# Optimization experiments

Hardware: AMD Instinct MI355X
Metric: run time of the kernel (lower is better)

Reference implementation:

```python
import jax, jax.numpy as jnp
import numpy as np

NUM_LAYERS = 3
INPUT_SIZE = 64
EMB = 128
NUM_CAT = 128          # must equal EMB for the W_e_proj assignment to shape-check
NUM_QUERIES = 1
INIT_SCALE = 0.02
KERNEL_PARAM = 1.0     # referenced-but-undefined in source; standard alpha=1
B = 16
N = 2048
D = INPUT_SIZE + 2 * EMB                 # 320, transformer embedding dim
F_IN = INPUT_SIZE + NUM_CAT + EMB        # 320, raw input feature dim


def setup_inputs() -> dict:
    key = jax.random.key(0)
    k = jax.random.split(key, 6)
    x = jax.random.normal(k[0], (B, F_IN, N), dtype=jnp.float32)
    embedding_matrix = jax.random.normal(k[1], (EMB, NUM_CAT), dtype=jnp.float32)
    W_Q = jax.random.normal(k[2], (NUM_LAYERS, 1, D, D), dtype=jnp.float32) * INIT_SCALE
    W_K = jax.random.normal(k[3], (NUM_LAYERS, 1, D, D), dtype=jnp.float32) * INIT_SCALE
    W_V = jax.random.normal(k[4], (NUM_LAYERS, 1, D, D), dtype=jnp.float32) * INIT_SCALE
    P = jax.random.normal(k[5], (NUM_LAYERS, 1, D, D), dtype=jnp.float32) * INIT_SCALE
    return {"x": x, "embedding_matrix": embedding_matrix,
            "W_Q": W_Q, "W_K": W_K, "W_V": W_V, "P": P}


def _build_We(embedding_matrix):
    W = jnp.zeros((D, F_IN), dtype=embedding_matrix.dtype)
    W = W.at[:INPUT_SIZE, :INPUT_SIZE].set(jnp.eye(INPUT_SIZE, dtype=W.dtype))
    W = W.at[D - EMB:, F_IN - EMB:].set(jnp.eye(EMB, dtype=W.dtype))
    # rows [input_size : D-emb], cols [input_size : F-num_categories]
    W = W.at[INPUT_SIZE:D - EMB, INPUT_SIZE:F_IN - NUM_CAT].set(embedding_matrix)
    return W


def reference(x, embedding_matrix, W_Q, W_K, W_V, P):
    W = _build_We(embedding_matrix)
    h = jnp.einsum('df,bfn->bdn', W, x)                        # [B, D, N]
    for nl in range(NUM_LAYERS):
        key = h[:, :, :-NUM_QUERIES]                           # include_query=False
        value = key
        query = h
        n_context = key.shape[-1]
        Q = jnp.einsum('id,bdm->bim', W_Q[nl, 0], query)       # [B, D, N]
        K = jnp.einsum('id,bdn->bin', W_K[nl, 0], key)         # [B, D, M]
        V = jnp.einsum('id,bdn->bin', W_V[nl, 0], value)       # [B, D, M]
        # linear kernel scores
        scores = KERNEL_PARAM * jnp.einsum('bim,bin->bmn', Q, K)  # [B, N, M]
        attn = jnp.einsum('bin,bmn->bim', V, scores) / n_context  # [B, D, N]
        h = h + jnp.einsum('ji,bim->bjm', P[nl, 0], attn)
    f = h[:, -EMB:, :]                                         # [B, EMB, N] (squeeze no-op for B>1)
    logits = jnp.einsum('bdn,dc->bnc', f, embedding_matrix)    # [B, N, C]
    predictions = jax.nn.softmax(logits, axis=-1)
    return logits, predictions
```

## Files before the change

kernel.cpp:

```cpp
#include <hip/hip_runtime.h>
#include <math.h>

typedef long long ll;
typedef unsigned int uint;
typedef unsigned short ushort;
typedef __attribute__((ext_vector_type(4))) float f32x4;
typedef __attribute__((ext_vector_type(8))) short bf16x8;

#define SZ 102400LL
#define RS 40960LL

__device__ inline void split2(float v, ushort& h, ushort& l)
{
    uint u = __float_as_uint(v);
    uint uh = u + (0x7FFFu + ((u >> 16) & 1u));
    h = (ushort)(uh >> 16);
    float hf = __uint_as_float((uint)h << 16);
    float d = v - hf;
    uint ud = __float_as_uint(d);
    l = (ushort)((ud + (0x7FFFu + ((ud >> 16) & 1u))) >> 16);
}
__device__ inline float us2f(ushort h, ushort l)
{
    return __uint_as_float((uint)h << 16) + __uint_as_float((uint)l << 16);
}

__global__ __launch_bounds__(256) void sp_k(
    const float* __restrict__ Wq, const float* __restrict__ Wk,
    const float* __restrict__ Wv, const float* __restrict__ P,
    const float* __restrict__ emb,
    ushort* __restrict__ WqTs, ushort* __restrict__ WkTs, ushort* __restrict__ WvTs,
    ushort* __restrict__ Ps, ushort* __restrict__ embs, ushort* __restrict__ embTs,
    float* __restrict__ q0)
{
    int bid = blockIdx.x, tid = threadIdx.x;
    if (bid < 225) {
        int m = bid / 25, t = bid % 25;
        const float* mats[3] = {Wq, Wk, Wv};
        ushort* dsts[3] = {WqTs, WkTs, WvTs};
        const float* src = mats[m / 3] + (ll)(m % 3) * SZ;
        ushort* dst = dsts[m / 3] + (ll)(m % 3) * SZ;
        int r0 = (t / 5) * 64, c0 = (t % 5) * 64;
        __shared__ float T[64][65];
        #pragma unroll
        for (int s = 0; s < 4; ++s) {
            int idx = s * 256 + tid;
            int r = idx >> 4, cq = (idx & 15) * 4;
            *(float4*)&T[r][cq] = *(const float4*)(src + (ll)(r0 + r) * 320 + c0 + cq);
        }
        __syncthreads();
        {
            int c = tid >> 2, kq = (tid & 3) * 16;
            bf16x8 h0, h1, l0, l1;
            #pragma unroll
            for (int u = 0; u < 8; ++u) {
                ushort h, l;
                split2(T[kq + u][c], h, l);     h0[u] = (short)h; l0[u] = (short)l;
                split2(T[kq + 8 + u][c], h, l); h1[u] = (short)h; l1[u] = (short)l;
            }
            ushort* dh = dst + (ll)(c0 + c) * 320 + r0 + kq;
            *(bf16x8*)dh = h0; *(bf16x8*)(dh + 8) = h1;
            *(bf16x8*)(dh + 3 * SZ) = l0; *(bf16x8*)(dh + 3 * SZ + 8) = l1;
        }
    } else if (bid < 375) {
        ll off = (ll)(bid - 225) * 2048 + tid * 8;
        float4 v0 = *(const float4*)(P + off);
        float4 v1 = *(const float4*)(P + off + 4);
        float vals[8] = {v0.x,v0.y,v0.z,v0.w,v1.x,v1.y,v1.z,v1.w};
        bf16x8 hv, lv;
        #pragma unroll
        for (int u = 0; u < 8; ++u) { ushort h,l; split2(vals[u],h,l);
                                      hv[u]=(short)h; lv[u]=(short)l; }
        *(bf16x8*)(Ps + off) = hv;
        *(bf16x8*)(Ps + off + 3 * SZ) = lv;
    } else if (bid < 383) {
        ll off = (ll)(bid - 375) * 2048 + tid * 8;
        float4 v0 = *(const float4*)(emb + off);
        float4 v1 = *(const float4*)(emb + off + 4);
        float vals[8] = {v0.x,v0.y,v0.z,v0.w,v1.x,v1.y,v1.z,v1.w};
        bf16x8 hv, lv;
        #pragma unroll
        for (int u = 0; u < 8; ++u) { ushort h,l; split2(vals[u],h,l);
                                      hv[u]=(short)h; lv[u]=(short)l; }
        *(bf16x8*)(embs + off) = hv;
        *(bf16x8*)(embs + off + 16384) = lv;
    } else if (bid < 387) {
        int t = bid - 383;
        int r0 = (t >> 1) * 64, c0 = (t & 1) * 64;
        __shared__ float T[64][65];
        {
            int r = tid >> 2, cq = (tid & 3) * 4;
            *(float4*)&T[r][cq]      = *(const float4*)(emb + (ll)(r0 + r) * 128 + c0 + cq);
            *(float4*)&T[r][cq + 16] = *(const float4*)(emb + (ll)(r0 + r) * 128 + c0 + cq + 16);
            *(float4*)&T[r][cq + 32] = *(const float4*)(emb + (ll)(r0 + r) * 128 + c0 + cq + 32);
            *(float4*)&T[r][cq + 48] = *(const float4*)(emb + (ll)(r0 + r) * 128 + c0 + cq + 48);
        }
        __syncthreads();
        {
            int c = tid >> 2, kq = (tid & 3) * 16;
            bf16x8 h0, h1, l0, l1;
            #pragma unroll
            for (int u = 0; u < 8; ++u) {
                ushort h, l;
                split2(T[kq + u][c], h, l);     h0[u]=(short)h; l0[u]=(short)l;
                split2(T[kq + 8 + u][c], h, l); h1[u]=(short)h; l1[u]=(short)l;
            }
            ushort* dh = embTs + (ll)(c0 + c) * 128 + r0 + kq;
            *(bf16x8*)dh = h0; *(bf16x8*)(dh + 8) = h1;
            *(bf16x8*)(dh + 16384) = l0; *(bf16x8*)(dh + 16384 + 8) = l1;
        }
    } else {
        ll base = (ll)(bid - 387) * 2048;
        #pragma unroll
        for (int s = 0; s < 8; ++s) {
            ll id = base + s * 256 + tid;
            int c = (int)(id / 320), i = (int)(id % 320);
            q0[id] = (i >= 192) ? emb[(ll)(i - 192) * 128 + c] : 0.f;
        }
    }
}

__global__ __launch_bounds__(256) void gram_mfma_k(const float* __restrict__ x,
                                                   float* __restrict__ part)
{
    int flat = blockIdx.x;
    int swz = (flat & 7) * 120 + (flat >> 3);
    int b = swz / 60;
    int rr = swz - b * 60;
    int p = rr / 15, t = rr - p * 15;
    int ti = 0, rem = t;
    while (rem >= 5 - ti) { rem -= 5 - ti; ++ti; }
    int tj = ti + rem;
    int i0 = ti * 64, j0 = tj * 64;
    bool diag = (ti == tj);
    const float* X = x + (ll)b * 320 * 2048;
    __shared__ __align__(16) ushort Ah[64 * 40], Al_[64 * 40], Bh[64 * 40], Bl_[64 * 40];
    int tid = threadIdx.x;
    int wv = tid >> 6, lane = tid & 63;
    int lr = lane & 15, kb = (lane >> 4) * 8;
    int cr = tid >> 2, ck = (tid & 3) * 8;
    f32x4 hh[4], hl[4], lh[4];
    f32x4 zz = {0.f, 0.f, 0.f, 0.f};
    #pragma unroll
    for (int f = 0; f < 4; ++f) { hh[f] = zz; hl[f] = zz; lh[f] = zz; }
    const ushort* BhS = diag ? Ah : Bh;
    const ushort* BlS = diag ? Al_ : Bl_;

    for (int it = 0; it < 16; ++it) {
        int kg0 = p * 512 + it * 32;
        {
            const float* src = X + (ll)(i0 + cr) * 2048 + kg0 + ck;
            float4 v0 = *(const float4*)src;
            float4 v1 = *(const float4*)(src + 4);
            float vals[8] = {v0.x,v0.y,v0.z,v0.w,v1.x,v1.y,v1.z,v1.w};
            if (kg0 + ck + 7 >= 2047) {
                #pragma unroll
                for (int u = 0; u < 8; ++u) if (kg0 + ck + u >= 2047) vals[u] = 0.f;
            }
            bf16x8 hv, lv;
            #pragma unroll
            for (int u = 0; u < 8; ++u) { ushort h, l; split2(vals[u], h, l);
                                          hv[u] = (short)h; lv[u] = (short)l; }
            *(bf16x8*)&Ah[cr * 40 + ck] = hv;
            *(bf16x8*)&Al_[cr * 40 + ck] = lv;
        }
        if (!diag) {
            const float* src = X + (ll)(j0 + cr) * 2048 + kg0 + ck;
            float4 v0 = *(const float4*)src;
            float4 v1 = *(const float4*)(src + 4);
            float vals[8] = {v0.x,v0.y,v0.z,v0.w,v1.x,v1.y,v1.z,v1.w};
            if (kg0 + ck + 7 >= 2047) {
                #pragma unroll
                for (int u = 0; u < 8; ++u) if (kg0 + ck + u >= 2047) vals[u] = 0.f;
            }
            bf16x8 hv, lv;
            #pragma unroll
            for (int u = 0; u < 8; ++u) { ushort h, l; split2(vals[u], h, l);
                                          hv[u] = (short)h; lv[u] = (short)l; }
            *(bf16x8*)&Bh[cr * 40 + ck] = hv;
            *(bf16x8*)&Bl_[cr * 40 + ck] = lv;
        }
        __syncthreads();
        bf16x8 ah = *(const bf16x8*)&Ah[(wv * 16 + lr) * 40 + kb];
        bf16x8 al = *(const bf16x8*)&Al_[(wv * 16 + lr) * 40 + kb];
        #pragma unroll
        for (int f = 0; f < 4; ++f) {
            bf16x8 bh_ = *(const bf16x8*)&BhS[(f * 16 + lr) * 40 + kb];
            bf16x8 bl_ = *(const bf16x8*)&BlS[(f * 16 + lr) * 40 + kb];
            hh[f] = __builtin_amdgcn_mfma_f32_16x16x32_bf16(ah, bh_, hh[f], 0, 0, 0);
            hl[f] = __builtin_amdgcn_mfma_f32_16x16x32_bf16(ah, bl_, hl[f], 0, 0, 0);
            lh[f] = __builtin_amdgcn_mfma_f32_16x16x32_bf16(al, bh_, lh[f], 0, 0, 0);
        }
        __syncthreads();
    }
    float* out = part + (((ll)p * 16 + b) * 15 + t) * 4096;
    int orow0 = wv * 16 + (lane >> 4) * 4;
    #pragma unroll
    for (int f = 0; f < 4; ++f) {
        int col = f * 16 + lr;
        #pragma unroll
        for (int r = 0; r < 4; ++r)
            out[(orow0 + r) * 64 + col] = hh[f][r] + hl[f][r] + lh[f][r];
    }
}

__global__ __launch_bounds__(256) void gram_red_k(const float* __restrict__ part,
                                                  ushort* __restrict__ GxS,
                                                  ushort* __restrict__ T1s)
{
    int bt = blockIdx.x;
    int b = bt / 15, t = bt % 15;
    int ti = 0, rem = t;
    while (rem >= 5 - ti) { rem -= 5 - ti; ++ti; }
    int tj = ti + rem;
    int i0 = ti * 64, j0 = tj * 64;
    int tid = threadIdx.x;
    int tx = tid & 15, rg = tid >> 4;
    bool wi = (ti == 0 || ti >= 3);
    bool wj = (tj == 0 || tj >= 3);
    ushort* Gb = GxS + (ll)b * SZ;
    ushort* Tsb = T1s + (ll)b * SZ;
    #pragma unroll
    for (int m = 0; m < 4; ++m) {
        int r = rg * 4 + m;
        float s[4] = {};
        for (int p = 0; p < 4; ++p) {
            const float* src = part + (((ll)p * 16 + b) * 15 + t) * 4096 + r * 64 + tx * 4;
            float4 v = *(const float4*)src;
            s[0]+=v.x; s[1]+=v.y; s[2]+=v.z; s[3]+=v.w;
        }
        #pragma unroll
        for (int u = 0; u < 4; ++u) {
            ushort h, l; split2(s[u], h, l);
            ll rd = (ll)(i0 + r) * 320 + j0 + tx * 4 + u;
            ll rt = (ll)(j0 + tx * 4 + u) * 320 + (i0 + r);
            Gb[rd] = h; Gb[rd + 16 * SZ] = l;
            Gb[rt] = h; Gb[rt + 16 * SZ] = l;
            if (wi) { Tsb[rd] = h; Tsb[rd + 16 * SZ] = l; }
            if (wj) { Tsb[rt] = h; Tsb[rt + 16 * SZ] = l; }
        }
    }
}

struct CJob {
    const ushort *Ah, *Bh;
    const void *Ci, *Ci2;
    float* C; ushort* Cs;
    ll aB, bB, ciB, ci2B, cB, csB;
    ll aLo, bLo, csLo, ciLo, ci2Lo;
    int aS, bS, ciS, ci2S, cS, csS;
    int K, tN, tpb, flags;
    int swzQ, swzR;
    float alpha;
};
struct CPack { CJob j[4]; };

__global__ __launch_bounds__(256) void mchain_k(CPack jp, int c0, int c1, int c2)
{
    int bid = blockIdx.x;
    int ji, local;
    if (bid < c0)      { ji = 0; local = bid; }
    else if (bid < c1) { ji = 1; local = bid - c0; }
    else if (bid < c2) { ji = 2; local = bid - c1; }
    else               { ji = 3; local = bid - c2; }
    CJob j = jp.j[ji];
    int xcd = local & 7, sidx = local >> 3;
    int base = (xcd < j.swzR) ? xcd * (j.swzQ + 1)
                              : j.swzR * (j.swzQ + 1) + (xcd - j.swzR) * j.swzQ;
    int swz = base + sidx;
    int bz = swz / j.tpb;
    int t = swz - bz * j.tpb;
    int i0 = (t / j.tN) * 64, j0 = (t % j.tN) * 64;
    int tid = threadIdx.x;
    int wv = tid >> 6, lane = tid & 63;
    int lr = lane & 15, kb = (lane >> 4) * 8;
    f32x4 hh[4], cx[4];
    f32x4 zz = {0.f,0.f,0.f,0.f};
    #pragma unroll
    for (int f = 0; f < 4; ++f) { hh[f] = zz; cx[f] = zz; }

    __shared__ __align__(16) ushort Bsh[2][2][2560];

    if (j.K > 0) {
        int srow = tid >> 2, skq = (tid & 3) * 8;
        const ushort* Bg = j.Bh + (ll)bz * j.bB + (ll)(j0 + srow) * j.bS + skq;
        const ushort* Ar = j.Ah + (ll)bz * j.aB + (ll)(i0 + wv * 16 + lr) * j.aS + kb;
        bf16x8 svh, svl, ah, al, ahn, aln;
        svh = *(const bf16x8*)Bg;
        svl = *(const bf16x8*)(Bg + j.bLo);
        *(bf16x8*)&Bsh[0][0][srow * 40 + skq] = svh;
        *(bf16x8*)&Bsh[0][1][srow * 40 + skq] = svl;
        ah = *(const bf16x8*)Ar;
        al = *(const bf16x8*)(Ar + j.aLo);
        __syncthreads();
        int nit = j.K >> 5;
        for (int it = 0; it < nit; ++it) {
            int cur = it & 1;
            bool more = (it + 1 < nit);
            if (more) {
                int k1 = (it + 1) << 5;
                svh = *(const bf16x8*)(Bg + k1);
                svl = *(const bf16x8*)(Bg + j.bLo + k1);
                ahn = *(const bf16x8*)(Ar + k1);
                aln = *(const bf16x8*)(Ar + j.aLo + k1);
            }
            #pragma unroll
            for (int f = 0; f < 4; ++f) {
                bf16x8 bh = *(const bf16x8*)&Bsh[cur][0][(f * 16 + lr) * 40 + kb];
                bf16x8 bl = *(const bf16x8*)&Bsh[cur][1][(f * 16 + lr) * 40 + kb];
                hh[f] = __builtin_amdgcn_mfma_f32_16x16x32_bf16(ah, bh, hh[f], 0, 0, 0);
                cx[f] = __builtin_amdgcn_mfma_f32_16x16x32_bf16(ah, bl, cx[f], 0, 0, 0);
                cx[f] = __builtin_amdgcn_mfma_f32_16x16x32_bf16(al, bh, cx[f], 0, 0, 0);
            }
            if (more) {
                *(bf16x8*)&Bsh[cur ^ 1][0][srow * 40 + skq] = svh;
                *(bf16x8*)&Bsh[cur ^ 1][1][srow * 40 + skq] = svl;
                ah = ahn; al = aln;
            }
            __syncthreads();
        }
    }
    const float* Cif = (const float*)j.Ci;
    const ushort* Ciu = (const ushort*)j.Ci;
    const float* Ci2f = (const float*)j.Ci2;
    const ushort* Ci2u = (const ushort*)j.Ci2;
    float* Cp = j.C + (ll)bz * j.cB;
    ushort* Csp = j.Cs + (ll)bz * j.csB;
    int r0 = i0 + wv * 16 + ((lane >> 4) << 2);
    #pragma unroll
    for (int f = 0; f < 4; ++f) {
        int col = j0 + f * 16 + lr;
        #pragma unroll
        for (int r = 0; r < 4; ++r) {
            int row = r0 + r;
            float v = j.alpha * (hh[f][r] + cx[f][r]);
            if (j.flags & 1)
                v += Cif[(ll)bz * j.ciB + (ll)row * j.ciS + col];
            if (j.flags & 32) {
                const ushort* p = Ciu + (ll)bz * j.ciB + (ll)row * j.ciS + col;
                v += us2f(p[0], p[j.ciLo]);
            }
            if (j.flags & 64) {
                const ushort* b2 = Ci2u + (ll)bz * j.ci2B;
                if (j.flags & 2) { const ushort* p = b2 + (ll)row * j.ci2S + col;
                                   v += us2f(p[0], p[j.ci2Lo]); }
                if (j.flags & 4) { const ushort* p = b2 + (ll)col * j.ci2S + row;
                                   v += us2f(p[0], p[j.ci2Lo]); }
            } else {
                if (j.flags & 2) v += Ci2f[(ll)bz * j.ci2B + (ll)row * j.ci2S + col];
                if (j.flags & 4) v += Ci2f[(ll)bz * j.ci2B + (ll)col * j.ci2S + row];
            }
            if (j.flags & 8) Cp[(ll)row * j.cS + col] = v;
            if (j.flags & 16) {
                ushort h, l; split2(v, h, l);
                ushort* p = Csp + (ll)row * j.csS + col;
                p[0] = h; p[j.csLo] = l;
            }
        }
    }
}

__global__ __launch_bounds__(256) void logits_mfma_k(const float* __restrict__ x,
                                                     const ushort* __restrict__ LBs,
                                                     float* __restrict__ logits,
                                                     float* __restrict__ pred)
{
    int b = blockIdx.y;
    int i0 = blockIdx.x * 64;
    const float* X = x + (ll)b * 320 * 2048;
    const ushort* LB = LBs + (ll)b * RS;
    __shared__ float Xs_[2][32][68];
    int tid = threadIdx.x;
    int wv = tid >> 6, lane = tid & 63;
    int lr = lane & 15, kb = (lane >> 4) * 8;
    int lkk = tid >> 3, lq = tid & 7;
    f32x4 hh[8], cx[8];
    f32x4 zz = {0.f,0.f,0.f,0.f};
    #pragma unroll
    for (int f = 0; f < 8; ++f) { hh[f] = zz; cx[f] = zz; }
    float4 p0, p1;
    auto glb = [&](int k0) {
        const float* s = X + (ll)(k0 + lkk) * 2048 + i0 + lq * 8;
        p0 = *(const float4*)s; p1 = *(const float4*)(s + 4);
    };
    auto stl = [&](int buf) {
        *(float4*)&Xs_[buf][lkk][lq * 8] = p0;
        *(float4*)&Xs_[buf][lkk][lq * 8 + 4] = p1;
    };
    glb(0); stl(0);
    __syncthreads();
    for (int it = 0; it < 10; ++it) {
        int cur = it & 1;
        if (it < 9) glb((it + 1) * 32);
        bf16x8 ah, al;
        #pragma unroll
        for (int u = 0; u < 8; ++u) {
            ushort h, l;
            split2(Xs_[cur][kb + u][wv * 16 + lr], h, l);
            ah[u] = (short)h; al[u] = (short)l;
        }
        #pragma unroll
        for (int f = 0; f < 8; ++f) {
            const ushort* Bp = LB + (ll)(f * 16 + lr) * 320 + it * 32 + kb;
            bf16x8 bh = *(const bf16x8*)Bp;
            bf16x8 bl = *(const bf16x8*)(Bp + 16 * RS);
            hh[f] = __builtin_amdgcn_mfma_f32_16x16x32_bf16(ah, bh, hh[f], 0, 0, 0);
            cx[f] = __builtin_amdgcn_mfma_f32_16x16x32_bf16(ah, bl, cx[f], 0, 0, 0);
            cx[f] = __builtin_amdgcn_mfma_f32_16x16x32_bf16(al, bh, cx[f], 0, 0, 0);
        }
        if (it < 9) stl(cur ^ 1);
        __syncthreads();
    }
    #pragma unroll
    for (int r = 0; r < 4; ++r) {
        int n = i0 + wv * 16 + ((lane >> 4) << 2) + r;
        float v[8];
        float mx = -1e30f;
        #pragma unroll
        for (int f = 0; f < 8; ++f) { v[f] = hh[f][r] + cx[f][r]; mx = fmaxf(mx, v[f]); }
        #pragma unroll
        for (int off = 8; off; off >>= 1) mx = fmaxf(mx, __shfl_xor(mx, off));
        float e[8], sm = 0.f;
        #pragma unroll
        for (int f = 0; f < 8; ++f) { e[f] = expf(v[f] - mx); sm += e[f]; }
        #pragma unroll
        for (int off = 8; off; off >>= 1) sm += __shfl_xor(sm, off);
        float inv = 1.f / sm;
        ll ro = ((ll)b * 2048 + n) * 128 + lr;
        #pragma unroll
        for (int f = 0; f < 8; ++f) {
            logits[ro + f * 16] = v[f];
            pred[ro + f * 16] = e[f] * inv;
        }
    }
}

extern "C" void kernel_launch(void* const* d_in, const int* in_sizes, int n_in,
                              void* d_out, int out_size, void* d_ws, size_t ws_size,
                              hipStream_t stream)
{
    const float* x   = (const float*)d_in[0];
    const float* emb = (const float*)d_in[1];
    const float* Wq  = (const float*)d_in[2];
    const float* Wk  = (const float*)d_in[3];
    const float* Wv  = (const float*)d_in[4];
    const float* P   = (const float*)d_in[5];

    float* logits = (float*)d_out;
    float* pred   = logits + (ll)16 * 2048 * 128;

    float* w = (float*)d_ws;
    auto takef = [&](ll n) { float* p = w; w += n; return p; };
    ushort* GxS  = (ushort*)takef(16 * SZ);
    ushort* T1s  = (ushort*)takef(16 * SZ);
    ushort* Gs   = (ushort*)takef(16 * SZ);
    ushort* As   = (ushort*)takef(16 * SZ);
    ushort* Us   = (ushort*)takef(16 * SZ);
    float*  ATsF = takef(48 * SZ);
    ushort* ATs  = (ushort*)ATsF;
    ushort* PVs  = (ushort*)takef(3 * SZ);
    ushort* KQTs = (ushort*)takef(3 * SZ);
    ushort* KQs  = (ushort*)takef(3 * SZ);
    ushort* Ps   = (ushort*)takef(3 * SZ);
    ushort* WqTs = (ushort*)takef(3 * SZ);
    ushort* WkTs = (ushort*)takef(3 * SZ);
    ushort* WvTs = (ushort*)takef(3 * SZ);
    ushort* embs = (ushort*)takef(16384);
    ushort* embTs= (ushort*)takef(16384);
    float*  q0f  = takef(RS);
    ushort* q1s  = (ushort*)takef(16 * RS);
    ushort* q2s  = (ushort*)takef(16 * RS);
    ushort* LBs  = (ushort*)takef(16 * RS);
    ushort* Xs   = GxS;
    ushort* Zts  = T1s;
    float*  part = ATsF;
    ushort* q3s  = q1s;
    const float cinv = 1.f / 2047.f;

    auto JB = [](const ushort* Ah, ll aB, int aS, ll aLo,
                 const ushort* Bh, ll bB, int bS, ll bLo,
                 int K, int tM, int tN, float alpha, int flags,
                 const void* Ci, ll ciB, int ciS, ll ciLo,
                 const void* Ci2, ll ci2B, int ci2S, ll ci2Lo,
                 float* C, ll cB, int cS,
                 ushort* Cs, ll csB, int csS, ll csLo) {
        CJob j;
        j.Ah = Ah; j.Bh = Bh;
        j.Ci = Ci; j.Ci2 = Ci2; j.C = C; j.Cs = Cs;
        j.aB = aB; j.bB = bB; j.ciB = ciB; j.ci2B = ci2B; j.cB = cB; j.csB = csB;
        j.aLo = aLo; j.bLo = bLo; j.csLo = csLo; j.ciLo = ciLo; j.ci2Lo = ci2Lo;
        j.aS = aS; j.bS = bS; j.ciS = ciS; j.ci2S = ci2S; j.cS = cS; j.csS = csS;
        j.K = K; j.tN = tN; j.tpb = tM * tN; j.flags = flags; j.alpha = alpha;
        j.swzQ = 0; j.swzR = 0;
        return j;
    };
    auto fire = [&](const CJob* js, const int* nb, int n) {
        CPack jp;
        int cum[4], tot = 0;
        for (int i = 0; i < 4; ++i) {
            jp.j[i] = js[i < n ? i : 0];
            if (i < n) { jp.j[i].swzQ = nb[i] >> 3; jp.j[i].swzR = nb[i] & 7; }
            tot += (i < n ? nb[i] : 0);
            cum[i] = tot;
        }
        mchain_k<<<tot, 256, 0, stream>>>(jp, cum[0], cum[1], cum[2]);
    };

    sp_k<<<407, 256, 0, stream>>>(Wq, Wk, Wv, P, emb,
                                  WqTs, WkTs, WvTs, Ps, embs, embTs, q0f);
    gram_mfma_k<<<960, 256, 0, stream>>>(x, part);
    gram_red_k<<<240, 256, 0, stream>>>(part, GxS, T1s);
    {
        CJob js[4] = {
            JB(embs, 0, 128, 16384,  GxS + 64, SZ, 320, 16*SZ,  128, 2, 5, 1.f, 16,
               0,0,0,0, 0,0,0,0,  0,0,0,  T1s + 64*320, SZ, 320, 16*SZ),
            JB(Ps, SZ, 320, 3*SZ,  WvTs, SZ, 320, 3*SZ,  320, 5, 5, 1.f, 16,
               0,0,0,0, 0,0,0,0,  0,0,0,  PVs, SZ, 320, 3*SZ),
            JB(WqTs, SZ, 320, 3*SZ,  WkTs, SZ, 320, 3*SZ,  320, 5, 5, 1.f, 16,
               0,0,0,0, 0,0,0,0,  0,0,0,  KQTs, SZ, 320, 3*SZ),
            JB(WkTs, SZ, 320, 3*SZ,  WqTs, SZ, 320, 3*SZ,  320, 5, 5, 1.f, 16,
               0,0,0,0, 0,0,0,0,  0,0,0,  KQs, SZ, 320, 3*SZ)};
        int nb[4] = {160, 75, 75, 75};
        fire(js, nb, 4);
    }
    {
        CJob js[3] = {
            JB(T1s + 64, SZ, 320, 16*SZ,  embs, 0, 128, 16384,  128, 5, 2, 1.f, 16,
               0,0,0,0, 0,0,0,0,  0,0,0,  Gs + 64, SZ, 320, 16*SZ),
            JB(0,0,0,0, 0,0,0,0,  0, 5, 1, 0.f, 32|16,
               T1s, SZ, 320, 16*SZ, 0,0,0,0,  0,0,0,  Gs, SZ, 320, 16*SZ),
            JB(0,0,0,0, 0,0,0,0,  0, 5, 2, 0.f, 32|16,
               T1s + 192, SZ, 320, 16*SZ, 0,0,0,0,  0,0,0,  Gs + 192, SZ, 320, 16*SZ)};
        int nb[3] = {160, 80, 160};
        fire(js, nb, 3);
    }
    for (int l = 0; l < 3; ++l) {
        const ushort* PVl = PVs + (ll)l * SZ;
        const ushort* KQTl = KQTs + (ll)l * SZ;
        const ushort* KQl = KQs + (ll)l * SZ;
        ushort* ATl = ATs + (ll)l * 16 * SZ;
        if (l < 2) {
            CJob s1[2] = {
                JB(PVl, 0, 320, 3*SZ,  Gs, SZ, 320, 16*SZ,  320, 5, 5, 1.f, 16,
                   0,0,0,0, 0,0,0,0,  0,0,0,  Xs, SZ, 320, 16*SZ),
                JB(Gs, SZ, 320, 16*SZ,  KQl, 0, 320, 3*SZ,  320, 5, 5, 1.f, 16,
                   0,0,0,0, 0,0,0,0,  0,0,0,  Zts, SZ, 320, 16*SZ)};
            int n1[2] = {400, 400};
            fire(s1, n1, 2);
            CJob s2[3] = {
                JB(Xs, SZ, 320, 16*SZ,  KQTl, 0, 320, 3*SZ,  320, 5, 5, cinv, 16,
                   0,0,0,0, 0,0,0,0,  0,0,0,  As, SZ, 320, 16*SZ),
                JB(KQTl, 0, 320, 3*SZ,  Xs, SZ, 320, 16*SZ,  320, 5, 5, cinv, 16,
                   0,0,0,0, 0,0,0,0,  0,0,0,  ATl, SZ, 320, 48*SZ),
                JB(Xs, SZ, 320, 16*SZ,  Zts, SZ, 320, 16*SZ,  320, 5, 5, cinv, 16,
                   0,0,0,0, 0,0,0,0,  0,0,0,  Us, SZ, 320, 16*SZ)};
            int n2[3] = {400, 400, 400};
            fire(s2, n2, 3);
            CJob s3[1] = {
                JB(Us, SZ, 320, 16*SZ,  As, SZ, 320, 16*SZ,  320, 5, 5, 1.f, 16|32|2|4|64,
                   Gs, SZ, 320, 16*SZ,  Us, SZ, 320, 16*SZ,  0,0,0,  Gs, SZ, 320, 16*SZ)};
            int n3[1] = {400};
            fire(s3, n3, 1);
        } else {
            CJob s1[1] = {
                JB(PVl, 0, 320, 3*SZ,  Gs, SZ, 320, 16*SZ,  320, 5, 5, 1.f, 16,
                   0,0,0,0, 0,0,0,0,  0,0,0,  Xs, SZ, 320, 16*SZ)};
            int n1[1] = {400};
            fire(s1, n1, 1);
            CJob s2[1] = {
                JB(KQTl, 0, 320, 3*SZ,  Xs, SZ, 320, 16*SZ,  320, 5, 5, cinv, 16,
                   0,0,0,0, 0,0,0,0,  0,0,0,  ATl, SZ, 320, 48*SZ)};
            int n2[1] = {400};
            fire(s2, n2, 1);
        }
    }
    {
        CJob js[1] = {
            JB(embTs, 0, 128, 16384,  ATs + 2*16*SZ + 192, SZ, 320, 48*SZ,  128, 2, 5, 1.f, 1|16,
               q0f, 0, 320, 0, 0,0,0,0,  0,0,0,  q1s, RS, 320, 16*RS)};
        int nb[1] = {160};
        fire(js, nb, 1);
    }
    {
        CJob js[1] = {
            JB(q1s, RS, 320, 16*RS,  ATs + 1*16*SZ, SZ, 320, 48*SZ,  320, 2, 5, 1.f, 32|16,
               q1s, RS, 320, 16*RS, 0,0,0,0,  0,0,0,  q2s, RS, 320, 16*RS)};
        int nb[1] = {160};
        fire(js, nb, 1);
    }
    {
        CJob js[1] = {
            JB(q2s, RS, 320, 16*RS,  ATs, SZ, 320, 48*SZ,  320, 2, 5, 1.f, 32|16,
               q2s, RS, 320, 16*RS, 0,0,0,0,  0,0,0,  q3s, RS, 320, 16*RS)};
        int nb[1] = {160};
        fire(js, nb, 1);
    }
    {
        CJob js[3] = {
            JB(q3s + 64, RS, 320, 16*RS,  embTs, 0, 128, 16384,  128, 2, 2, 1.f, 16,
               0,0,0,0, 0,0,0,0,  0,0,0,  LBs + 64, RS, 320, 16*RS),
            JB(0,0,0,0, 0,0,0,0,  0, 2, 1, 0.f, 32|16,
               q3s, RS, 320, 16*RS, 0,0,0,0,  0,0,0,  LBs, RS, 320, 16*RS),
            JB(0,0,0,0, 0,0,0,0,  0, 2, 2, 0.f, 32|16,
               q3s + 192, RS, 320, 16*RS, 0,0,0,0,  0,0,0,  LBs + 192, RS, 320, 16*RS)};
        int nb[3] = {64, 32, 64};
        fire(js, nb, 3);
    }
    logits_mfma_k<<<dim3(32, 16), 256, 0, stream>>>(x, LBs, logits, pred);
}
```

Measured before the change: 320.6 us.

## Fuse gram and weight-split kernels; retile logits kernel into 32-row blocks with cross-wave softmax

New measurement: 315.4 us. Within noise of the previous version (-1.6%).

```diff
diff --git a/kernel.cpp b/kernel.cpp
--- a/kernel.cpp
+++ b/kernel.cpp
@@ -25,7 +25,8 @@
     return __uint_as_float((uint)h << 16) + __uint_as_float((uint)l << 16);
 }
 
-__global__ __launch_bounds__(256) void sp_k(
+__global__ __launch_bounds__(256) void gram_sp_k(
+    const float* __restrict__ x, float* __restrict__ part,
     const float* __restrict__ Wq, const float* __restrict__ Wk,
     const float* __restrict__ Wv, const float* __restrict__ P,
     const float* __restrict__ emb,
@@ -33,7 +34,94 @@
     ushort* __restrict__ Ps, ushort* __restrict__ embs, ushort* __restrict__ embTs,
     float* __restrict__ q0)
 {
-    int bid = blockIdx.x, tid = threadIdx.x;
+    __shared__ __align__(16) char smem[20480];
+    int bid0 = blockIdx.x, tid = threadIdx.x;
+    if (bid0 < 960) {
+        ushort* Ah  = (ushort*)smem;
+        ushort* Al_ = Ah + 2560;
+        ushort* Bh  = Al_ + 2560;
+        ushort* Bl_ = Bh + 2560;
+        int flat = bid0;
+        int swz = (flat & 7) * 120 + (flat >> 3);
+        int b = swz / 60;
+        int rr = swz - b * 60;
+        int p = rr / 15, t = rr - p * 15;
+        int ti = 0, rem = t;
+        while (rem >= 5 - ti) { rem -= 5 - ti; ++ti; }
+        int tj = ti + rem;
+        int i0 = ti * 64, j0 = tj * 64;
+        bool diag = (ti == tj);
+        const float* X = x + (ll)b * 320 * 2048;
+        int wv = tid >> 6, lane = tid & 63;
+        int lr = lane & 15, kb = (lane >> 4) * 8;
+        int cr = tid >> 2, ck = (tid & 3) * 8;
+        f32x4 hh[4], hl[4], lh[4];
+        f32x4 zz = {0.f, 0.f, 0.f, 0.f};
+        #pragma unroll
+        for (int f = 0; f < 4; ++f) { hh[f] = zz; hl[f] = zz; lh[f] = zz; }
+        const ushort* BhS = diag ? Ah : Bh;
+        const ushort* BlS = diag ? Al_ : Bl_;
+
+        for (int it = 0; it < 16; ++it) {
+            int kg0 = p * 512 + it * 32;
+            {
+                const float* src = X + (ll)(i0 + cr) * 2048 + kg0 + ck;
+                float4 v0 = *(const float4*)src;
+                float4 v1 = *(const float4*)(src + 4);
+                float vals[8] = {v0.x,v0.y,v0.z,v0.w,v1.x,v1.y,v1.z,v1.w};
+                if (kg0 + ck + 7 >= 2047) {
+                    #pragma unroll
+                    for (int u = 0; u < 8; ++u) if (kg0 + ck + u >= 2047) vals[u] = 0.f;
+                }
+                bf16x8 hv, lv;
+                #pragma unroll
+                for (int u = 0; u < 8; ++u) { ushort h, l; split2(vals[u], h, l);
+                                              hv[u] = (short)h; lv[u] = (short)l; }
+                *(bf16x8*)&Ah[cr * 40 + ck] = hv;
+                *(bf16x8*)&Al_[cr * 40 + ck] = lv;
+            }
+            if (!diag) {
+                const float* src = X + (ll)(j0 + cr) * 2048 + kg0 + ck;
+                float4 v0 = *(const float4*)src;
+                float4 v1 = *(const float4*)(src + 4);
+                float vals[8] = {v0.x,v0.y,v0.z,v0.w,v1.x,v1.y,v1.z,v1.w};
+                if (kg0 + ck + 7 >= 2047) {
+                    #pragma unroll
+                    for (int u = 0; u < 8; ++u) if (kg0 + ck + u >= 2047) vals[u] = 0.f;
+                }
+                bf16x8 hv, lv;
+                #pragma unroll
+                for (int u = 0; u < 8; ++u) { ushort h, l; split2(vals[u], h, l);
+                                              hv[u] = (short)h; lv[u] = (short)l; }
+                *(bf16x8*)&Bh[cr * 40 + ck] = hv;
+                *(bf16x8*)&Bl_[cr * 40 + ck] = lv;
+            }
+            __syncthreads();
+            bf16x8 ah = *(const bf16x8*)&Ah[(wv * 16 + lr) * 40 + kb];
+            bf16x8 al = *(const bf16x8*)&Al_[(wv * 16 + lr) * 40 + kb];
+            #pragma unroll
+            for (int f = 0; f < 4; ++f) {
+                bf16x8 bh_ = *(const bf16x8*)&BhS[(f * 16 + lr) * 40 + kb];
+                bf16x8 bl_ = *(const bf16x8*)&BlS[(f * 16 + lr) * 40 + kb];
+                hh[f] = __builtin_amdgcn_mfma_f32_16x16x32_bf16(ah, bh_, hh[f], 0, 0, 0);
+                hl[f] = __builtin_amdgcn_mfma_f32_16x16x32_bf16(ah, bl_, hl[f], 0, 0, 0);
+                lh[f] = __builtin_amdgcn_mfma_f32_16x16x32_bf16(al, bh_, lh[f], 0, 0, 0);
+            }
+            __syncthreads();
+        }
+        float* out = part + (((ll)p * 16 + b) * 15 + t) * 4096;
+        int orow0 = wv * 16 + (lane >> 4) * 4;
+        #pragma unroll
+        for (int f = 0; f < 4; ++f) {
+            int col = f * 16 + lr;
+            #pragma unroll
+            for (int r = 0; r < 4; ++r)
+                out[(orow0 + r) * 64 + col] = hh[f][r] + hl[f][r] + lh[f][r];
+        }
+        return;
+    }
+    int bid = bid0 - 960;
+    float (*T)[65] = (float(*)[65])smem;
     if (bid < 225) {
         int m = bid / 25, t = bid % 25;
         const float* mats[3] = {Wq, Wk, Wv};
@@ -41,7 +129,6 @@
         const float* src = mats[m / 3] + (ll)(m % 3) * SZ;
         ushort* dst = dsts[m / 3] + (ll)(m % 3) * SZ;
         int r0 = (t / 5) * 64, c0 = (t % 5) * 64;
-        __shared__ float T[64][65];
         #pragma unroll
         for (int s = 0; s < 4; ++s) {
             int idx = s * 256 + tid;
@@ -87,7 +174,6 @@
     } else if (bid < 387) {
         int t = bid - 383;
         int r0 = (t >> 1) * 64, c0 = (t & 1) * 64;
-        __shared__ float T[64][65];
         {
             int r = tid >> 2, cq = (tid & 3) * 4;
             *(float4*)&T[r][cq]      = *(const float4*)(emb + (ll)(r0 + r) * 128 + c0 + cq);
@@ -117,90 +203,6 @@
             int c = (int)(id / 320), i = (int)(id % 320);
             q0[id] = (i >= 192) ? emb[(ll)(i - 192) * 128 + c] : 0.f;
         }
-    }
-}
-
-__global__ __launch_bounds__(256) void gram_mfma_k(const float* __restrict__ x,
-                                                   float* __restrict__ part)
-{
-    int flat = blockIdx.x;
-    int swz = (flat & 7) * 120 + (flat >> 3);
-    int b = swz / 60;
-    int rr = swz - b * 60;
-    int p = rr / 15, t = rr - p * 15;
-    int ti = 0, rem = t;
-    while (rem >= 5 - ti) { rem -= 5 - ti; ++ti; }
-    int tj = ti + rem;
-    int i0 = ti * 64, j0 = tj * 64;
-    bool diag = (ti == tj);
-    const float* X = x + (ll)b * 320 * 2048;
-    __shared__ __align__(16) ushort Ah[64 * 40], Al_[64 * 40], Bh[64 * 40], Bl_[64 * 40];
-    int tid = threadIdx.x;
-    int wv = tid >> 6, lane = tid & 63;
-    int lr = lane & 15, kb = (lane >> 4) * 8;
-    int cr = tid >> 2, ck = (tid & 3) * 8;
-    f32x4 hh[4], hl[4], lh[4];
-    f32x4 zz = {0.f, 0.f, 0.f, 0.f};
-    #pragma unroll
-    for (int f = 0; f < 4; ++f) { hh[f] = zz; hl[f] = zz; lh[f] = zz; }
-    const ushort* BhS = diag ? Ah : Bh;
-    const ushort* BlS = diag ? Al_ : Bl_;
-
-    for (int it = 0; it < 16; ++it) {
-        int kg0 = p * 512 + it * 32;
-        {
-            const float* src = X + (ll)(i0 + cr) * 2048 + kg0 + ck;
-            float4 v0 = *(const float4*)src;
-            float4 v1 = *(const float4*)(src + 4);
-            float vals[8] = {v0.x,v0.y,v0.z,v0.w,v1.x,v1.y,v1.z,v1.w};
-            if (kg0 + ck + 7 >= 2047) {
-                #pragma unroll
-                for (int u = 0; u < 8; ++u) if (kg0 + ck + u >= 2047) vals[u] = 0.f;
-            }
-            bf16x8 hv, lv;
-            #pragma unroll
-            for (int u = 0; u < 8; ++u) { ushort h, l; split2(vals[u], h, l);
-                                          hv[u] = (short)h; lv[u] = (short)l; }
-            *(bf16x8*)&Ah[cr * 40 + ck] = hv;
-            *(bf16x8*)&Al_[cr * 40 + ck] = lv;
-        }
-        if (!diag) {
-            const float* src = X + (ll)(j0 + cr) * 2048 + kg0 + ck;
-            float4 v0 = *(const float4*)src;
-            float4 v1 = *(const float4*)(src + 4);
-            float vals[8] = {v0.x,v0.y,v0.z,v0.w,v1.x,v1.y,v1.z,v1.w};
-            if (kg0 + ck + 7 >= 2047) {
-                #pragma unroll
-                for (int u = 0; u < 8; ++u) if (kg0 + ck + u >= 2047) vals[u] = 0.f;
-            }
-            bf16x8 hv, lv;
-            #pragma unroll
-            for (int u = 0; u < 8; ++u) { ushort h, l; split2(vals[u], h, l);
-                                          hv[u] = (short)h; lv[u] = (short)l; }
-            *(bf16x8*)&Bh[cr * 40 + ck] = hv;
-            *(bf16x8*)&Bl_[cr * 40 + ck] = lv;
-        }
-        __syncthreads();
-        bf16x8 ah = *(const bf16x8*)&Ah[(wv * 16 + lr) * 40 + kb];
-        bf16x8 al = *(const bf16x8*)&Al_[(wv * 16 + lr) * 40 + kb];
-        #pragma unroll
-        for (int f = 0; f < 4; ++f) {
-            bf16x8 bh_ = *(const bf16x8*)&BhS[(f * 16 + lr) * 40 + kb];
-            bf16x8 bl_ = *(const bf16x8*)&BlS[(f * 16 + lr) * 40 + kb];
-            hh[f] = __builtin_amdgcn_mfma_f32_16x16x32_bf16(ah, bh_, hh[f], 0, 0, 0);
-            hl[f] = __builtin_amdgcn_mfma_f32_16x16x32_bf16(ah, bl_, hl[f], 0, 0, 0);
-            lh[f] = __builtin_amdgcn_mfma_f32_16x16x32_bf16(al, bh_, lh[f], 0, 0, 0);
-        }
-        __syncthreads();
-    }
-    float* out = part + (((ll)p * 16 + b) * 15 + t) * 4096;
-    int orow0 = wv * 16 + (lane >> 4) * 4;
-    #pragma unroll
-    for (int f = 0; f < 4; ++f) {
-        int col = f * 16 + lr;
-        #pragma unroll
-        for (int r = 0; r < 4; ++r)
-            out[(orow0 + r) * 64 + col] = hh[f][r] + hl[f][r] + lh[f][r];
     }
 }
 
@@ -365,27 +367,30 @@
                                                      float* __restrict__ logits,
                                                      float* __restrict__ pred)
 {
-    int b = blockIdx.y;
-    int i0 = blockIdx.x * 64;
+    int flat = blockIdx.x;
+    int swzb = (flat & 7) * 128 + (flat >> 3);
+    int b = swzb >> 6;
+    int i0 = (swzb & 63) * 32;
     const float* X = x + (ll)b * 320 * 2048;
     const ushort* LB = LBs + (ll)b * RS;
-    __shared__ float Xs_[2][32][68];
+    __shared__ float Xs_[2][32][33];
+    __shared__ float pmL[2][32], psL[2][32];
     int tid = threadIdx.x;
     int wv = tid >> 6, lane = tid & 63;
-    int lr = lane & 15, kb = (lane >> 4) * 8;
-    int lkk = tid >> 3, lq = tid & 7;
-    f32x4 hh[8], cx[8];
+    int lr = lane & 15, g = lane >> 4, kb = g * 8;
+    int rowg = (wv & 1) * 16, ch = wv >> 1, colh = ch * 64;
+    int lkk = tid >> 3, lq = (tid & 7) * 4;
+    f32x4 hh[4], cx[4];
     f32x4 zz = {0.f,0.f,0.f,0.f};
     #pragma unroll
-    for (int f = 0; f < 8; ++f) { hh[f] = zz; cx[f] = zz; }
-    float4 p0, p1;
+    for (int f = 0; f < 4; ++f) { hh[f] = zz; cx[f] = zz; }
+    float4 pa;
     auto glb = [&](int k0) {
-        const float* s = X + (ll)(k0 + lkk) * 2048 + i0 + lq * 8;
-        p0 = *(const float4*)s; p1 = *(const float4*)(s + 4);
+        pa = *(const float4*)(X + (ll)(k0 + lkk) * 2048 + i0 + lq);
     };
     auto stl = [&](int buf) {
-        *(float4*)&Xs_[buf][lkk][lq * 8] = p0;
-        *(float4*)&Xs_[buf][lkk][lq * 8 + 4] = p1;
+        float* p = &Xs_[buf][lkk][lq];
+        p[0] = pa.x; p[1] = pa.y; p[2] = pa.z; p[3] = pa.w;
     };
     glb(0); stl(0);
     __syncthreads();
@@ -396,12 +401,12 @@
         #pragma unroll
         for (int u = 0; u < 8; ++u) {
             ushort h, l;
-            split2(Xs_[cur][kb + u][wv * 16 + lr], h, l);
+            split2(Xs_[cur][kb + u][rowg + lr], h, l);
             ah[u] = (short)h; al[u] = (short)l;
         }
         #pragma unroll
-        for (int f = 0; f < 8; ++f) {
-            const ushort* Bp = LB + (ll)(f * 16 + lr) * 320 + it * 32 + kb;
+        for (int f = 0; f < 4; ++f) {
+            const ushort* Bp = LB + (ll)(colh + f * 16 + lr) * 320 + it * 32 + kb;
             bf16x8 bh = *(const bf16x8*)Bp;
             bf16x8 bl = *(const bf16x8*)(Bp + 16 * RS);
             hh[f] = __builtin_amdgcn_mfma_f32_16x16x32_bf16(ah, bh, hh[f], 0, 0, 0);
@@ -411,26 +416,41 @@
         if (it < 9) stl(cur ^ 1);
         __syncthreads();
     }
+    float v[4][4];
+    #pragma unroll
+    for (int r = 0; r < 4; ++r)
+        #pragma unroll
+        for (int f = 0; f < 4; ++f) v[r][f] = hh[f][r] + cx[f][r];
     #pragma unroll
     for (int r = 0; r < 4; ++r) {
-        int n = i0 + wv * 16 + ((lane >> 4) << 2) + r;
-        float v[8];
-        float mx = -1e30f;
-        #pragma unroll
-        for (int f = 0; f < 8; ++f) { v[f] = hh[f][r] + cx[f][r]; mx = fmaxf(mx, v[f]); }
-        #pragma unroll
-        for (int off = 8; off; off >>= 1) mx = fmaxf(mx, __shfl_xor(mx, off));
-        float e[8], sm = 0.f;
-        #pragma unroll
-        for (int f = 0; f < 8; ++f) { e[f] = expf(v[f] - mx); sm += e[f]; }
-        #pragma unroll
-        for (int off = 8; off; off >>= 1) sm += __shfl_xor(sm, off);
-        float inv = 1.f / sm;
-        ll ro = ((ll)b * 2048 + n) * 128 + lr;
-        #pragma unroll
-        for (int f = 0; f < 8; ++f) {
-            logits[ro + f * 16] = v[f];
-            pred[ro + f * 16] = e[f] * inv;
+        float m = fmaxf(fmaxf(v[r][0], v[r][1]), fmaxf(v[r][2], v[r][3]));
+        #pragma unroll
+        for (int off = 8; off; off >>= 1) m = fmaxf(m, __shfl_xor(m, off));
+        if (lr == 0) pmL[ch][rowg + g * 4 + r] = m;
+    }
+    __syncthreads();
+    float ev[4][4];
+    #pragma unroll
+    for (int r = 0; r < 4; ++r) {
+        int blr = rowg + g * 4 + r;
+        float mx = fmaxf(pmL[0][blr], pmL[1][blr]);
+        float s = 0.f;
+        #pragma unroll
+        for (int f = 0; f < 4; ++f) { ev[r][f] = expf(v[r][f] - mx); s += ev[r][f]; }
+        #pragma unroll
+        for (int off = 8; off; off >>= 1) s += __shfl_xor(s, off);
+        if (lr == 0) psL[ch][blr] = s;
+    }
+    __syncthreads();
+    #pragma unroll
+    for (int r = 0; r < 4; ++r) {
+        int blr = rowg + g * 4 + r;
+        float inv = 1.f / (psL[0][blr] + psL[1][blr]);
+        ll ro = ((ll)b * 2048 + i0 + blr) * 128 + colh + lr;
+        #pragma unroll
+        for (int f = 0; f < 4; ++f) {
+            logits[ro + f * 16] = v[r][f];
+            pred[ro + f * 16] = ev[r][f] * inv;
         }
     }
 }
@@ -506,9 +526,8 @@
         mchain_k<<<tot, 256, 0, stream>>>(jp, cum[0], cum[1], cum[2]);
     };
 
-    sp_k<<<407, 256, 0, stream>>>(Wq, Wk, Wv, P, emb,
-                                  WqTs, WkTs, WvTs, Ps, embs, embTs, q0f);
-    gram_mfma_k<<<960, 256, 0, stream>>>(x, part);
+    gram_sp_k<<<1367, 256, 0, stream>>>(x, part, Wq, Wk, Wv, P, emb,
+                                        WqTs, WkTs, WvTs, Ps, embs, embTs, q0f);
     gram_red_k<<<240, 256, 0, stream>>>(part, GxS, T1s);
     {
         CJob js[4] = {
@@ -606,5 +625,5 @@
         int nb[3] = {64, 32, 64};
         fire(js, nb, 3);
     }
-    logits_mfma_k<<<dim3(32, 16), 256, 0, stream>>>(x, LBs, logits, pred);
+    logits_mfma_k<<<1024, 256, 0, stream>>>(x, LBs, logits, pred);
 }
```
